# Optimization experiments

Hardware: AMD Instinct MI355X
Metric: run time of the kernel (lower is better)

## Reference

```python
import jax, jax.numpy as jnp
import numpy as np

N_PROJECT = 100000
N_COMPANY = 50000
N_EDGES = 1000000
INPUT_DIM = 256
HIDDEN_DIM = 128
NUM_LAYERS = 2
EPS = 1e-12


def setup_inputs() -> dict:
    key = jax.random.key(0)
    ks = jax.random.split(key, 10)
    return {
        "x_project": jax.random.normal(ks[0], (N_PROJECT, INPUT_DIM), jnp.float32),
        "x_company": jax.random.normal(ks[1], (N_COMPANY, INPUT_DIM), jnp.float32),
        "W_project": jax.random.normal(ks[2], (INPUT_DIM, HIDDEN_DIM), jnp.float32) * 0.05,
        "b_project": jax.random.normal(ks[3], (HIDDEN_DIM,), jnp.float32) * 0.05,
        "W_company": jax.random.normal(ks[4], (INPUT_DIM, HIDDEN_DIM), jnp.float32) * 0.05,
        "b_company": jax.random.normal(ks[5], (HIDDEN_DIM,), jnp.float32) * 0.05,
        "pc_src": jax.random.randint(ks[6], (N_EDGES,), 0, N_PROJECT, jnp.int32),
        "pc_dst": jax.random.randint(ks[7], (N_EDGES,), 0, N_COMPANY, jnp.int32),
        "cp_src": jax.random.randint(ks[8], (N_EDGES,), 0, N_COMPANY, jnp.int32),
        "cp_dst": jax.random.randint(ks[9], (N_EDGES,), 0, N_PROJECT, jnp.int32),
    }


def _rel_aggregate(x_src, row, col, num_src, num_dst):
    # D_src^-1/2 A D_dst^-1/2 normalized gather-scale-scatter_add for one relation.
    ones = jnp.ones(row.shape[0], jnp.float32)
    deg_s = jax.ops.segment_sum(ones, row, num_segments=num_src)
    deg_d = jax.ops.segment_sum(ones, col, num_segments=num_dst)
    inv_s = jnp.where(deg_s > 0, deg_s ** -0.5, 0.0)
    inv_d = jnp.where(deg_d > 0, deg_d ** -0.5, 0.0)
    w = inv_s[row] * inv_d[col]                      # [E]
    msg = x_src[row] * w[:, None]                    # [E, H]
    return jax.ops.segment_sum(msg, col, num_segments=num_dst)  # [num_dst, H]


def reference(x_project, x_company, W_project, b_project, W_company, b_company,
              pc_src, pc_dst, cp_src, cp_dst):
    h_p = x_project @ W_project + b_project          # [Np, H]
    h_c = x_company @ W_company + b_company          # [Nc, H]
    acc_p, acc_c = h_p, h_c
    for _ in range(NUM_LAYERS):
        new_p = _rel_aggregate(h_c, cp_src, cp_dst, N_COMPANY, N_PROJECT)
        new_c = _rel_aggregate(h_p, pc_src, pc_dst, N_PROJECT, N_COMPANY)
        h_p, h_c = new_p, new_c
        acc_p = acc_p + h_p
        acc_c = acc_c + h_c
    scale = 1.0 / (NUM_LAYERS + 1)
    out_p = acc_p * scale
    out_c = acc_c * scale
    # F.normalize(p=2, dim=-1)
    out_p = out_p / jnp.maximum(jnp.linalg.norm(out_p, axis=-1, keepdims=True), EPS)
    out_c = out_c / jnp.maximum(jnp.linalg.norm(out_c, axis=-1, keepdims=True), EPS)
    return out_p, out_c
```

## Files before the change

### kernel.cpp

```cpp
#include <hip/hip_runtime.h>
#include <hip/hip_bf16.h>
#include <math.h>

#define HD 128
#define KD 256
#define CAP 64
#define CAPA 96
#define BA 128

typedef __attribute__((ext_vector_type(8))) short bf16x8;
typedef __attribute__((ext_vector_type(4))) float f32x4;

__device__ __forceinline__ unsigned short bfbits(float x) {
    __hip_bfloat16 h = __float2bfloat16(x);
    return *(unsigned short*)&h;
}
__device__ __forceinline__ unsigned int pack_bf2(float a, float b) {
    __hip_bfloat162 h;
    h.x = __float2bfloat16(a);
    h.y = __float2bfloat16(b);
    return *(unsigned int*)&h;
}
__device__ __forceinline__ float2 unpack_bf2(unsigned int u) {
    __hip_bfloat162 h = *(__hip_bfloat162*)&u;
    return __bfloat1622float2(h);
}
__device__ __forceinline__ bf16x8 cvt8(float4 a, float4 b) {
    bf16x8 r;
    r[0] = (short)bfbits(a.x); r[1] = (short)bfbits(a.y);
    r[2] = (short)bfbits(a.z); r[3] = (short)bfbits(a.w);
    r[4] = (short)bfbits(b.x); r[5] = (short)bfbits(b.y);
    r[6] = (short)bfbits(b.z); r[7] = (short)bfbits(b.w);
    return r;
}

__launch_bounds__(256)
__global__ void phaseA(
        const int* __restrict__ cps, const int* __restrict__ cpd,
        int* __restrict__ db0, int* __restrict__ sb0, int* cntD0, int* cntS0,
        const int* __restrict__ pcs, const int* __restrict__ pcd,
        int* __restrict__ db1, int* __restrict__ sb1, int* cntD1, int* cntS1,
        int E, int G0, int G1,
        const float* __restrict__ WA, unsigned short* __restrict__ WtA,
        const float* __restrict__ WB, unsigned short* __restrict__ WtB) {
    __shared__ int curD[256], curS[256];
    const int b = blockIdx.x;
    if (b >= 2 * BA) {
        int idx = (b - 2 * BA) * 256 + threadIdx.x;
        const float* W = (idx < KD * HD) ? WA : WB;
        unsigned short* Wt = (idx < KD * HD) ? WtA : WtB;
        int id = idx & (KD * HD - 1);
        int j = id & 7, lane = (id >> 3) & 63, nt = (id >> 9) & 7, kc = id >> 12;
        int k = kc * 32 + (lane >> 4) * 8 + j;
        int c = nt * 16 + (lane & 15);
        Wt[id] = bfbits(W[k * HD + c]);
        return;
    }
    const int rel = b >> 7;
    const int ib  = b & (BA - 1);
    const int* src = rel ? pcs : cps;
    const int* dst = rel ? pcd : cpd;
    int* db   = rel ? db1 : db0;
    int* sb   = rel ? sb1 : sb0;
    int* cntD = rel ? cntD1 : cntD0;
    int* cntS = rel ? cntS1 : cntS0;
    const int shD = rel ? 8 : 9;
    const int shS = rel ? 9 : 8;
    const int GD  = rel ? G1 : G0;
    const int GS  = rel ? G0 : G1;

    for (int i = threadIdx.x; i < 256; i += 256) { curD[i] = 0; curS[i] = 0; }
    __syncthreads();

    const int chunk = (E + BA - 1) / BA;
    const int e0 = ib * chunk;
    const int e1 = (e0 + chunk < E) ? e0 + chunk : E;
    for (int e = e0 + (int)threadIdx.x; e < e1; e += 256) {
        const int s = src[e];
        const int d = dst[e];
        const int gd = d >> shD;
        const int pd = atomicAdd(&curD[gd], 1);
        if (pd < CAPA)
            db[((size_t)(ib * GD + gd)) * CAPA + pd] = ((d - (gd << shD)) << 17) | s;
        const int gs = s >> shS;
        const int ps = atomicAdd(&curS[gs], 1);
        if (ps < CAPA)
            sb[((size_t)(ib * GS + gs)) * CAPA + ps] = s;
    }
    __syncthreads();
    for (int g = threadIdx.x; g < GD; g += 256)
        cntD[ib * GD + g] = (curD[g] < CAPA) ? curD[g] : CAPA;
    for (int g = threadIdx.x; g < GS; g += 256)
        cntS[ib * GS + g] = (curS[g] < CAPA) ? curS[g] : CAPA;
}

__device__ __forceinline__ void gemm_body(
        char* smem, const float* __restrict__ X, const unsigned short* __restrict__ Wt,
        const float* __restrict__ bias, unsigned short* __restrict__ out0,
        int M, int tile) {
    float (*eps)[16][68] = (float (*)[16][68])smem;

    const int t = threadIdx.x;
    const int lane = t & 63;
    const int w = t >> 6;
    const int lr = lane & 15;
    const int kb = lane >> 4;
    const int rbase = tile * 128;

    f32x4 acc[2][8];
    #pragma unroll
    for (int nt = 0; nt < 8; ++nt) {
        float bv = bias[nt * 16 + lr];
        acc[0][nt] = (f32x4){bv, bv, bv, bv};
        acc[1][nt] = (f32x4){bv, bv, bv, bv};
    }

    const float4* X4 = (const float4*)X;
    const int r0 = rbase + w * 32 + lr;
    const int r1 = r0 + 16;
    const size_t rr0 = (size_t)((r0 < M) ? r0 : 0) * 64 + kb * 2;
    const size_t rr1 = (size_t)((r1 < M) ? r1 : 0) * 64 + kb * 2;

    float4 xf[2][4];
    #pragma unroll
    for (int s = 0; s < 2; ++s) {
        xf[s][0] = X4[rr0 + s * 8];
        xf[s][1] = X4[rr0 + s * 8 + 1];
        xf[s][2] = X4[rr1 + s * 8];
        xf[s][3] = X4[rr1 + s * 8 + 1];
    }

    #pragma unroll
    for (int kc = 0; kc < 8; ++kc) {
        const int s = kc & 1;
        bf16x8 a0 = cvt8(xf[s][0], xf[s][1]);
        bf16x8 a1 = cvt8(xf[s][2], xf[s][3]);
        if (kc < 6) {
            xf[s][0] = X4[rr0 + (kc + 2) * 8];
            xf[s][1] = X4[rr0 + (kc + 2) * 8 + 1];
            xf[s][2] = X4[rr1 + (kc + 2) * 8];
            xf[s][3] = X4[rr1 + (kc + 2) * 8 + 1];
        }
        const unsigned short* wb = Wt + ((size_t)(kc * 8) * 64 + lane) * 8;
        #pragma unroll
        for (int nt = 0; nt < 8; ++nt) {
            bf16x8 b = *(const bf16x8*)(wb + (size_t)nt * 512);
            acc[0][nt] = __builtin_amdgcn_mfma_f32_16x16x32_bf16(a0, b, acc[0][nt], 0, 0, 0);
            acc[1][nt] = __builtin_amdgcn_mfma_f32_16x16x32_bf16(a1, b, acc[1][nt], 0, 0, 0);
        }
    }

    const int er = lane >> 2;
    const int ec = lane & 3;
    #pragma unroll
    for (int mt = 0; mt < 2; ++mt) {
        #pragma unroll
        for (int hf = 0; hf < 2; ++hf) {
            __syncthreads();
            #pragma unroll
            for (int nt = 0; nt < 4; ++nt)
                #pragma unroll
                for (int reg = 0; reg < 4; ++reg)
                    eps[w][kb * 4 + reg][nt * 16 + lr] = acc[mt][hf * 4 + nt][reg];
            __syncthreads();
            const int g = rbase + w * 32 + mt * 16 + er;
            if (g < M) {
                #pragma unroll
                for (int i = 0; i < 4; ++i) {
                    const int f4c = ec + i * 4;
                    float4 v = *(const float4*)&eps[w][er][f4c * 4];
                    uint2 u;
                    u.x = pack_bf2(v.x, v.y);
                    u.y = pack_bf2(v.z, v.w);
                    *(uint2*)(out0 + (size_t)g * HD + hf * 64 + f4c * 4) = u;
                }
            }
        }
    }
}

__launch_bounds__(256, 4)
__global__ void phaseB(
        const int* __restrict__ db0, const int* cntD0, int* csr0, int* degs0,
        const int* __restrict__ db1, const int* cntD1, int* csr1, int* degs1,
        const int* __restrict__ sb0, const int* cntS0, int* hist0,
        const int* __restrict__ sb1, const int* cntS1, int* hist1,
        int G0, int G1, int Np, int Nc,
        const float* Xp, const unsigned short* WtP, const float* bp,
        unsigned short* h0p, int GP,
        const float* Xc, const unsigned short* WtC, const float* bc,
        unsigned short* h0c) {
    __shared__ __align__(16) char smem[17408];
    int* lcur = (int*)smem;
    const int r = blockIdx.x;
    const int nLight = 2 * (G0 + G1);

    if (r < nLight) {
        int g, sh, GD, M;
        const int *bkt, *cnt;
        int *outp, *degs;
        bool isCSR;
        if (r < G0) {
            g = r; sh = 9; GD = G0; M = Np; bkt = db0; cnt = cntD0;
            outp = csr0; degs = degs0; isCSR = true;
        } else if (r < G0 + G1) {
            g = r - G0; sh = 8; GD = G1; M = Nc; bkt = db1; cnt = cntD1;
            outp = csr1; degs = degs1; isCSR = true;
        } else if (r < G0 + 2 * G1) {
            g = r - G0 - G1; sh = 8; GD = G1; M = Nc; bkt = sb0; cnt = cntS0;
            outp = hist0; degs = hist0; isCSR = false;
        } else {
            g = r - G0 - 2 * G1; sh = 9; GD = G0; M = Np; bkt = sb1; cnt = cntS1;
            outp = hist1; degs = hist1; isCSR = false;
        }
        const int base = g << sh;
        const int rows = ((M - base) < (1 << sh)) ? (M - base) : (1 << sh);
        for (int i = threadIdx.x; i < rows; i += 256) lcur[i] = 0;
        __syncthreads();
        const int total = BA * CAPA;
        if (isCSR) {
            for (int idx = threadIdx.x; idx < total; idx += 256) {
                const int bb = idx / CAPA;
                const int i  = idx - bb * CAPA;
                if (i < cnt[bb * GD + g]) {
                    const unsigned int v = ((const unsigned int*)bkt)[(size_t)(bb * GD + g) * CAPA + i];
                    const int s = (int)(v & 0x1FFFF);
                    const int dloc = (int)(v >> 17);
                    const int p = atomicAdd(&lcur[dloc], 1);
                    if (p < CAP) outp[((size_t)(base + dloc) << 6) + p] = s;
                }
            }
        } else {
            for (int idx = threadIdx.x; idx < total; idx += 256) {
                const int bb = idx / CAPA;
                const int i  = idx - bb * CAPA;
                if (i < cnt[bb * GD + g]) {
                    const int s = bkt[(size_t)(bb * GD + g) * CAPA + i];
                    atomicAdd(&lcur[s - base], 1);
                }
            }
        }
        __syncthreads();
        for (int i = threadIdx.x; i < rows; i += 256)
            degs[base + i] = (lcur[i] < CAP) ? lcur[i] : (isCSR ? CAP : lcur[i]);
        return;
    }

    const int gFlat = r - nLight;
    if (gFlat < GP)
        gemm_body(smem, Xp, WtP, bp, h0p, Np, gFlat);
    else
        gemm_body(smem, Xc, WtC, bc, h0c, Nc, gFlat - GP);
}

__device__ __forceinline__ void agg_gather(const int* __restrict__ degs,
                                           const int* __restrict__ ssrc,
                                           const int* __restrict__ scnt,
                                           const unsigned short* __restrict__ hsrc,
                                           int row, int lane, int q, int cl,
                                           float4& accA, float4& accB) {
    const int deg = degs[row];
    accA = make_float4(0.f, 0.f, 0.f, 0.f);
    accB = make_float4(0.f, 0.f, 0.f, 0.f);
    if (deg > 0) {
        const float id = rsqrtf((float)deg);
        const int n = (deg < CAP) ? deg : CAP;
        int sl = 0; float wl = 0.f;
        if (lane < n) {
            sl = ssrc[((size_t)row << 6) + lane];
            wl = rsqrtf((float)scnt[sl]);
        }
        for (int jj = 0; jj < n; jj += 4) {
            const int j = jj + q;
            const int s = __shfl(sl, j);
            const float wt = __shfl(wl, j) * id;
            const uint4 u = *(const uint4*)(hsrc + (size_t)s * HD + cl * 8);
            const float2 f0 = unpack_bf2(u.x);
            const float2 f1 = unpack_bf2(u.y);
            const float2 f2 = unpack_bf2(u.z);
            const float2 f3 = unpack_bf2(u.w);
            accA.x = fmaf(f0.x, wt, accA.x);
            accA.y = fmaf(f0.y, wt, accA.y);
            accA.z = fmaf(f1.x, wt, accA.z);
            accA.w = fmaf(f1.y, wt, accA.w);
            accB.x = fmaf(f2.x, wt, accB.x);
            accB.y = fmaf(f2.y, wt, accB.y);
            accB.z = fmaf(f3.x, wt, accB.z);
            accB.w = fmaf(f3.y, wt, accB.w);
        }
    }
    accA.x += __shfl_xor(accA.x, 16); accA.y += __shfl_xor(accA.y, 16);
    accA.z += __shfl_xor(accA.z, 16); accA.w += __shfl_xor(accA.w, 16);
    accB.x += __shfl_xor(accB.x, 16); accB.y += __shfl_xor(accB.y, 16);
    accB.z += __shfl_xor(accB.z, 16); accB.w += __shfl_xor(accB.w, 16);
    accA.x += __shfl_xor(accA.x, 32); accA.y += __shfl_xor(accA.y, 32);
    accA.z += __shfl_xor(accA.z, 32); accA.w += __shfl_xor(accA.w, 32);
    accB.x += __shfl_xor(accB.x, 32); accB.y += __shfl_xor(accB.y, 32);
    accB.z += __shfl_xor(accB.z, 32); accB.w += __shfl_xor(accB.w, 32);
}

__global__ void agg_dual(const int* degsA, const int* ssrcA, const int* scntA,
                         const unsigned short* hsrcA, unsigned short* hdstA, int MA,
                         const int* degsB, const int* ssrcB, const int* scntB,
                         const unsigned short* hsrcB, unsigned short* hdstB, int MB) {
    const int bA = (MA + 3) / 4;
    const int lane = threadIdx.x & 63;
    const int q  = lane >> 4;
    const int cl = lane & 15;
    int row;
    const int *degs, *ssrc, *scnt;
    const unsigned short* hsrc; unsigned short* hdst; int M;
    if ((int)blockIdx.x < bA) {
        row = blockIdx.x * 4 + (threadIdx.x >> 6);
        degs = degsA; ssrc = ssrcA; scnt = scntA; hsrc = hsrcA; hdst = hdstA; M = MA;
    } else {
        row = (blockIdx.x - bA) * 4 + (threadIdx.x >> 6);
        degs = degsB; ssrc = ssrcB; scnt = scntB; hsrc = hsrcB; hdst = hdstB; M = MB;
    }
    if (row >= M) return;
    float4 accA, accB;
    agg_gather(degs, ssrc, scnt, hsrc, row, lane, q, cl, accA, accB);
    if (q == 0) {
        uint4 u;
        u.x = pack_bf2(accA.x, accA.y);
        u.y = pack_bf2(accA.z, accA.w);
        u.z = pack_bf2(accB.x, accB.y);
        u.w = pack_bf2(accB.z, accB.w);
        *(uint4*)(hdst + (size_t)row * HD + cl * 8) = u;
    }
}

__global__ void agg_norm_dual(const int* degsA, const int* ssrcA, const int* scntA,
                              const unsigned short* hsrcA, const unsigned short* h0A,
                              const unsigned short* h1A, float* outA, int MA,
                              const int* degsB, const int* ssrcB, const int* scntB,
                              const unsigned short* hsrcB, const unsigned short* h0B,
                              const unsigned short* h1B, float* outB, int MB) {
    const int bA = (MA + 3) / 4;
    const int lane = threadIdx.x & 63;
    const int q  = lane >> 4;
    const int cl = lane & 15;
    int row;
    const int *degs, *ssrc, *scnt;
    const unsigned short *hsrc, *h0, *h1; float* outp; int M;
    if ((int)blockIdx.x < bA) {
        row = blockIdx.x * 4 + (threadIdx.x >> 6);
        degs = degsA; ssrc = ssrcA; scnt = scntA; hsrc = hsrcA;
        h0 = h0A; h1 = h1A; outp = outA; M = MA;
    } else {
        row = (blockIdx.x - bA) * 4 + (threadIdx.x >> 6);
        degs = degsB; ssrc = ssrcB; scnt = scntB; hsrc = hsrcB;
        h0 = h0B; h1 = h1B; outp = outB; M = MB;
    }
    if (row >= M) return;
    float4 accA, accB;
    agg_gather(degs, ssrc, scnt, hsrc, row, lane, q, cl, accA, accB);

    float2 h2;
    if (q == 0)      h2 = make_float2(accA.x, accA.y);
    else if (q == 1) h2 = make_float2(accA.z, accA.w);
    else if (q == 2) h2 = make_float2(accB.x, accB.y);
    else             h2 = make_float2(accB.z, accB.w);

    const int c = cl * 8 + q * 2;
    const size_t base = (size_t)row * HD + c;
    float2 h0v = unpack_bf2(*(const unsigned int*)(h0 + base));
    float2 h1v = unpack_bf2(*(const unsigned int*)(h1 + base));
    const float sc = 1.0f / 3.0f;
    float vx = (h0v.x + h1v.x + h2.x) * sc;
    float vy = (h0v.y + h1v.y + h2.y) * sc;
    float ss = vx * vx + vy * vy;
    #pragma unroll
    for (int off = 1; off < 64; off <<= 1) ss += __shfl_xor(ss, off);
    float inv = 1.0f / fmaxf(sqrtf(ss), 1e-12f);
    *(float2*)(outp + base) = make_float2(vx * inv, vy * inv);
}

extern "C" void kernel_launch(void* const* d_in, const int* in_sizes, int n_in,
                              void* d_out, int out_size, void* d_ws, size_t ws_size,
                              hipStream_t stream) {
    const float* x_p = (const float*)d_in[0];
    const float* x_c = (const float*)d_in[1];
    const float* W_p = (const float*)d_in[2];
    const float* b_p = (const float*)d_in[3];
    const float* W_c = (const float*)d_in[4];
    const float* b_c = (const float*)d_in[5];
    const int* pcs = (const int*)d_in[6];
    const int* pcd = (const int*)d_in[7];
    const int* cps = (const int*)d_in[8];
    const int* cpd = (const int*)d_in[9];

    const int Np = in_sizes[0] / KD;
    const int Nc = in_sizes[1] / KD;
    const int E  = in_sizes[6];

    const int G0 = (Np + 511) >> 9;
    const int G1 = (Nc + 255) >> 8;

    int* scp = (int*)d_ws;
    int* spc = scp + ((size_t)Np << 6);
    int* c_cps = spc + ((size_t)Nc << 6);
    int* c_pcs = c_cps + Nc;
    int* c_cpd = c_pcs + Np;
    int* c_pcd = c_cpd + Np;
    unsigned short* bufP0 = (unsigned short*)(c_pcd + Nc);
    unsigned short* bufP1 = bufP0 + (size_t)Np * HD;
    unsigned short* bufC0 = bufP1 + (size_t)Np * HD;
    unsigned short* bufC1 = bufC0 + (size_t)Nc * HD;
    unsigned short* WtP = bufC1 + (size_t)Nc * HD;
    unsigned short* WtC = WtP + KD * HD;
    int* db0 = (int*)(WtC + KD * HD);
    int* db1 = db0 + (size_t)BA * G0 * CAPA;
    int* sb0 = db1 + (size_t)BA * G1 * CAPA;
    int* sb1 = sb0 + (size_t)BA * G1 * CAPA;
    int* cntD0 = sb1 + (size_t)BA * G0 * CAPA;
    int* cntD1 = cntD0 + BA * G0;
    int* cntS0 = cntD1 + BA * G1;
    int* cntS1 = cntS0 + BA * G1;

    float* outP = (float*)d_out;
    float* outC = outP + (size_t)Np * HD;

    phaseA<<<2 * BA + 256, 256, 0, stream>>>(
        cps, cpd, db0, sb0, cntD0, cntS0,
        pcs, pcd, db1, sb1, cntD1, cntS1,
        E, G0, G1, W_p, WtP, W_c, WtC);

    const int GP = (Np + 127) / 128;
    const int GC = (Nc + 127) / 128;
    phaseB<<<2 * (G0 + G1) + GP + GC, 256, 0, stream>>>(
        db0, cntD0, scp, c_cpd,
        db1, cntD1, spc, c_pcd,
        sb0, cntS0, c_cps,
        sb1, cntS1, c_pcs,
        G0, G1, Np, Nc,
        x_p, WtP, b_p, bufP0, GP,
        x_c, WtC, b_c, bufC0);

    const int bP = (Np + 3) / 4, bC = (Nc + 3) / 4;

    agg_dual<<<bP + bC, 256, 0, stream>>>(
        c_cpd, scp, c_cps, bufC0, bufP1, Np,
        c_pcd, spc, c_pcs, bufP0, bufC1, Nc);

    agg_norm_dual<<<bP + bC, 256, 0, stream>>>(
        c_cpd, scp, c_cps, bufC1, bufP0, bufP1, outP, Np,
        c_pcd, spc, c_pcs, bufP1, bufC0, bufC1, outC, Nc);
}
```

Baseline: 326.4 us.

## Stage full bf16 weight matrix in LDS and prefetch all X rows up front

The GEMM body now copies the entire 256x128 bf16 weight matrix (64 KB) into shared memory per block and reads MFMA B operands from LDS instead of global/L2. All eight K-chunks of X are loaded into registers before the MFMA loop, replacing the two-stage rolling prefetch. Shared memory grows to 64 KB and launch bounds drop to 2 blocks per CU, trading occupancy (also for the light bucket-processing blocks in the same kernel) and register pressure for fewer global weight reads.

```diff
diff --git a/kernel.cpp b/kernel.cpp
--- a/kernel.cpp
+++ b/kernel.cpp
@@ -98,6 +98,8 @@
         char* smem, const float* __restrict__ X, const unsigned short* __restrict__ Wt,
         const float* __restrict__ bias, unsigned short* __restrict__ out0,
         int M, int tile) {
+    uint4* lds4 = (uint4*)smem;
+    const unsigned short* lsh = (const unsigned short*)smem;
     float (*eps)[16][68] = (float (*)[16][68])smem;
 
     const int t = threadIdx.x;
@@ -107,44 +109,41 @@
     const int kb = lane >> 4;
     const int rbase = tile * 128;
 
-    f32x4 acc[2][8];
-    #pragma unroll
-    for (int nt = 0; nt < 8; ++nt) {
-        float bv = bias[nt * 16 + lr];
-        acc[0][nt] = (f32x4){bv, bv, bv, bv};
-        acc[1][nt] = (f32x4){bv, bv, bv, bv};
-    }
+    const uint4* Wg4 = (const uint4*)Wt;
+    #pragma unroll
+    for (int i = 0; i < 16; ++i) { int q = t + i * 256; lds4[q] = Wg4[q]; }
 
     const float4* X4 = (const float4*)X;
     const int r0 = rbase + w * 32 + lr;
     const int r1 = r0 + 16;
     const size_t rr0 = (size_t)((r0 < M) ? r0 : 0) * 64 + kb * 2;
     const size_t rr1 = (size_t)((r1 < M) ? r1 : 0) * 64 + kb * 2;
-
-    float4 xf[2][4];
-    #pragma unroll
-    for (int s = 0; s < 2; ++s) {
-        xf[s][0] = X4[rr0 + s * 8];
-        xf[s][1] = X4[rr0 + s * 8 + 1];
-        xf[s][2] = X4[rr1 + s * 8];
-        xf[s][3] = X4[rr1 + s * 8 + 1];
-    }
-
+    float4 xf[8][4];
     #pragma unroll
     for (int kc = 0; kc < 8; ++kc) {
-        const int s = kc & 1;
-        bf16x8 a0 = cvt8(xf[s][0], xf[s][1]);
-        bf16x8 a1 = cvt8(xf[s][2], xf[s][3]);
-        if (kc < 6) {
-            xf[s][0] = X4[rr0 + (kc + 2) * 8];
-            xf[s][1] = X4[rr0 + (kc + 2) * 8 + 1];
-            xf[s][2] = X4[rr1 + (kc + 2) * 8];
-            xf[s][3] = X4[rr1 + (kc + 2) * 8 + 1];
-        }
-        const unsigned short* wb = Wt + ((size_t)(kc * 8) * 64 + lane) * 8;
+        xf[kc][0] = X4[rr0 + kc * 8];
+        xf[kc][1] = X4[rr0 + kc * 8 + 1];
+        xf[kc][2] = X4[rr1 + kc * 8];
+        xf[kc][3] = X4[rr1 + kc * 8 + 1];
+    }
+
+    f32x4 acc[2][8];
+    #pragma unroll
+    for (int nt = 0; nt < 8; ++nt) {
+        float bv = bias[nt * 16 + lr];
+        acc[0][nt] = (f32x4){bv, bv, bv, bv};
+        acc[1][nt] = (f32x4){bv, bv, bv, bv};
+    }
+
+    __syncthreads();
+
+    #pragma unroll
+    for (int kc = 0; kc < 8; ++kc) {
+        bf16x8 a0 = cvt8(xf[kc][0], xf[kc][1]);
+        bf16x8 a1 = cvt8(xf[kc][2], xf[kc][3]);
         #pragma unroll
         for (int nt = 0; nt < 8; ++nt) {
-            bf16x8 b = *(const bf16x8*)(wb + (size_t)nt * 512);
+            bf16x8 b = *(const bf16x8*)&lsh[(((kc * 8 + nt) * 64) + lane) * 8];
             acc[0][nt] = __builtin_amdgcn_mfma_f32_16x16x32_bf16(a0, b, acc[0][nt], 0, 0, 0);
             acc[1][nt] = __builtin_amdgcn_mfma_f32_16x16x32_bf16(a1, b, acc[1][nt], 0, 0, 0);
         }
@@ -179,7 +178,7 @@
     }
 }
 
-__launch_bounds__(256, 4)
+__launch_bounds__(256, 2)
 __global__ void phaseB(
         const int* __restrict__ db0, const int* cntD0, int* csr0, int* degs0,
         const int* __restrict__ db1, const int* cntD1, int* csr1, int* degs1,
@@ -190,7 +189,7 @@
         unsigned short* h0p, int GP,
         const float* Xc, const unsigned short* WtC, const float* bc,
         unsigned short* h0c) {
-    __shared__ __align__(16) char smem[17408];
+    __shared__ __align__(16) char smem[65536];
     int* lcur = (int*)smem;
     const int r = blockIdx.x;
     const int nLight = 2 * (G0 + G1);
```

After: 322.6 us (median of 3 runs). About the same (-1.2%).

## Overlap projection GEMM with edge bucketing and stage CSR rows in LDS

Applied to the files above, without the earlier changes.

The projection GEMM moves out of the CSR-build kernel into the edge-bucketing kernel, so the dense matmul runs alongside the atomic bucketing work. Weight conversion becomes its own small kernel that runs first. CSR build is now a separate kernel that assembles each 256-row group's neighbour lists in a 64 KB shared-memory tile and writes them out with coalesced 16-byte stores. Both relations now use a uniform 256-row bucket granularity, and the layer-1 feature buffers reuse the bucket scratch memory. In exchange, the per-row neighbour cap drops from 64 to 63, there is one extra launch, and the large LDS footprint limits csrbuild occupancy.

```diff
diff --git a/kernel.cpp b/kernel.cpp
--- a/kernel.cpp
+++ b/kernel.cpp
@@ -34,64 +34,19 @@
     return r;
 }
 
-__launch_bounds__(256)
-__global__ void phaseA(
-        const int* __restrict__ cps, const int* __restrict__ cpd,
-        int* __restrict__ db0, int* __restrict__ sb0, int* cntD0, int* cntS0,
-        const int* __restrict__ pcs, const int* __restrict__ pcd,
-        int* __restrict__ db1, int* __restrict__ sb1, int* cntD1, int* cntS1,
-        int E, int G0, int G1,
-        const float* __restrict__ WA, unsigned short* __restrict__ WtA,
-        const float* __restrict__ WB, unsigned short* __restrict__ WtB) {
-    __shared__ int curD[256], curS[256];
-    const int b = blockIdx.x;
-    if (b >= 2 * BA) {
-        int idx = (b - 2 * BA) * 256 + threadIdx.x;
-        const float* W = (idx < KD * HD) ? WA : WB;
-        unsigned short* Wt = (idx < KD * HD) ? WtA : WtB;
-        int id = idx & (KD * HD - 1);
-        int j = id & 7, lane = (id >> 3) & 63, nt = (id >> 9) & 7, kc = id >> 12;
-        int k = kc * 32 + (lane >> 4) * 8 + j;
-        int c = nt * 16 + (lane & 15);
-        Wt[id] = bfbits(W[k * HD + c]);
-        return;
-    }
-    const int rel = b >> 7;
-    const int ib  = b & (BA - 1);
-    const int* src = rel ? pcs : cps;
-    const int* dst = rel ? pcd : cpd;
-    int* db   = rel ? db1 : db0;
-    int* sb   = rel ? sb1 : sb0;
-    int* cntD = rel ? cntD1 : cntD0;
-    int* cntS = rel ? cntS1 : cntS0;
-    const int shD = rel ? 8 : 9;
-    const int shS = rel ? 9 : 8;
-    const int GD  = rel ? G1 : G0;
-    const int GS  = rel ? G0 : G1;
-
-    for (int i = threadIdx.x; i < 256; i += 256) { curD[i] = 0; curS[i] = 0; }
-    __syncthreads();
-
-    const int chunk = (E + BA - 1) / BA;
-    const int e0 = ib * chunk;
-    const int e1 = (e0 + chunk < E) ? e0 + chunk : E;
-    for (int e = e0 + (int)threadIdx.x; e < e1; e += 256) {
-        const int s = src[e];
-        const int d = dst[e];
-        const int gd = d >> shD;
-        const int pd = atomicAdd(&curD[gd], 1);
-        if (pd < CAPA)
-            db[((size_t)(ib * GD + gd)) * CAPA + pd] = ((d - (gd << shD)) << 17) | s;
-        const int gs = s >> shS;
-        const int ps = atomicAdd(&curS[gs], 1);
-        if (ps < CAPA)
-            sb[((size_t)(ib * GS + gs)) * CAPA + ps] = s;
-    }
-    __syncthreads();
-    for (int g = threadIdx.x; g < GD; g += 256)
-        cntD[ib * GD + g] = (curD[g] < CAPA) ? curD[g] : CAPA;
-    for (int g = threadIdx.x; g < GS; g += 256)
-        cntS[ib * GS + g] = (curS[g] < CAPA) ? curS[g] : CAPA;
+__global__ void convW2(const float* __restrict__ WA, unsigned short* __restrict__ WtA,
+                       const float* __restrict__ WB, unsigned short* __restrict__ WtB) {
+    int idx = blockIdx.x * 256 + threadIdx.x;
+    const float* W = (idx < KD * HD) ? WA : WB;
+    unsigned short* Wt = (idx < KD * HD) ? WtA : WtB;
+    int id = idx & (KD * HD - 1);
+    int j    = id & 7;
+    int lane = (id >> 3) & 63;
+    int nt   = (id >> 9) & 7;
+    int kc   = id >> 12;
+    int k = kc * 32 + (lane >> 4) * 8 + j;
+    int c = nt * 16 + (lane & 15);
+    Wt[id] = bfbits(W[k * HD + c]);
 }
 
 __device__ __forceinline__ void gemm_body(
@@ -180,77 +135,128 @@
 }
 
 __launch_bounds__(256, 4)
-__global__ void phaseB(
+__global__ void fusedAG(
+        const int* __restrict__ cps, const int* __restrict__ cpd,
+        int* __restrict__ db0, int* __restrict__ sb0, int* cntD0, int* cntS0,
+        const int* __restrict__ pcs, const int* __restrict__ pcd,
+        int* __restrict__ db1, int* __restrict__ sb1, int* cntD1, int* cntS1,
+        int E, int G0, int G1,
+        const float* Xp, const unsigned short* WtP, const float* bp,
+        unsigned short* h0p, int Np, int GP,
+        const float* Xc, const unsigned short* WtC, const float* bc,
+        unsigned short* h0c, int Nc) {
+    __shared__ __align__(16) char smem[17408];
+    const int b = blockIdx.x;
+    if (b < 2 * BA) {
+        int* curD = (int*)smem;
+        int* curS = curD + 512;
+        const int rel = b >> 7;
+        const int ib  = b & (BA - 1);
+        const int* src = rel ? pcs : cps;
+        const int* dst = rel ? pcd : cpd;
+        int* db   = rel ? db1 : db0;
+        int* sb   = rel ? sb1 : sb0;
+        int* cntD = rel ? cntD1 : cntD0;
+        int* cntS = rel ? cntS1 : cntS0;
+        const int GD  = rel ? G1 : G0;
+        const int GS  = rel ? G0 : G1;
+
+        for (int i = threadIdx.x; i < 512; i += 256) { curD[i] = 0; curS[i] = 0; }
+        __syncthreads();
+
+        const int chunk = (E + BA - 1) / BA;
+        const int e0 = ib * chunk;
+        const int e1 = (e0 + chunk < E) ? e0 + chunk : E;
+        for (int e = e0 + (int)threadIdx.x; e < e1; e += 256) {
+            const int s = src[e];
+            const int d = dst[e];
+            const int gd = d >> 8;
+            const int pd = atomicAdd(&curD[gd], 1);
+            if (pd < CAPA)
+                db[((size_t)(ib * GD + gd)) * CAPA + pd] = ((d & 255) << 17) | s;
+            const int gs = s >> 8;
+            const int ps = atomicAdd(&curS[gs], 1);
+            if (ps < CAPA)
+                sb[((size_t)(ib * GS + gs)) * CAPA + ps] = s;
+        }
+        __syncthreads();
+        for (int g = threadIdx.x; g < GD; g += 256)
+            cntD[ib * GD + g] = (curD[g] < CAPA) ? curD[g] : CAPA;
+        for (int g = threadIdx.x; g < GS; g += 256)
+            cntS[ib * GS + g] = (curS[g] < CAPA) ? curS[g] : CAPA;
+        return;
+    }
+    const int gFlat = b - 2 * BA;
+    if (gFlat < GP)
+        gemm_body(smem, Xp, WtP, bp, h0p, Np, gFlat);
+    else
+        gemm_body(smem, Xc, WtC, bc, h0c, Nc, gFlat - GP);
+}
+
+__launch_bounds__(256)
+__global__ void csrbuild(
         const int* __restrict__ db0, const int* cntD0, int* csr0, int* degs0,
         const int* __restrict__ db1, const int* cntD1, int* csr1, int* degs1,
         const int* __restrict__ sb0, const int* cntS0, int* hist0,
         const int* __restrict__ sb1, const int* cntS1, int* hist1,
-        int G0, int G1, int Np, int Nc,
-        const float* Xp, const unsigned short* WtP, const float* bp,
-        unsigned short* h0p, int GP,
-        const float* Xc, const unsigned short* WtC, const float* bc,
-        unsigned short* h0c) {
-    __shared__ __align__(16) char smem[17408];
-    int* lcur = (int*)smem;
+        int G0, int G1, int Np, int Nc) {
+    __shared__ int rows[256 * 64];
     const int r = blockIdx.x;
-    const int nLight = 2 * (G0 + G1);
-
-    if (r < nLight) {
-        int g, sh, GD, M;
-        const int *bkt, *cnt;
-        int *outp, *degs;
-        bool isCSR;
-        if (r < G0) {
-            g = r; sh = 9; GD = G0; M = Np; bkt = db0; cnt = cntD0;
-            outp = csr0; degs = degs0; isCSR = true;
-        } else if (r < G0 + G1) {
-            g = r - G0; sh = 8; GD = G1; M = Nc; bkt = db1; cnt = cntD1;
-            outp = csr1; degs = degs1; isCSR = true;
-        } else if (r < G0 + 2 * G1) {
-            g = r - G0 - G1; sh = 8; GD = G1; M = Nc; bkt = sb0; cnt = cntS0;
-            outp = hist0; degs = hist0; isCSR = false;
-        } else {
-            g = r - G0 - 2 * G1; sh = 9; GD = G0; M = Np; bkt = sb1; cnt = cntS1;
-            outp = hist1; degs = hist1; isCSR = false;
-        }
-        const int base = g << sh;
-        const int rows = ((M - base) < (1 << sh)) ? (M - base) : (1 << sh);
-        for (int i = threadIdx.x; i < rows; i += 256) lcur[i] = 0;
-        __syncthreads();
-        const int total = BA * CAPA;
-        if (isCSR) {
-            for (int idx = threadIdx.x; idx < total; idx += 256) {
-                const int bb = idx / CAPA;
-                const int i  = idx - bb * CAPA;
-                if (i < cnt[bb * GD + g]) {
-                    const unsigned int v = ((const unsigned int*)bkt)[(size_t)(bb * GD + g) * CAPA + i];
-                    const int s = (int)(v & 0x1FFFF);
-                    const int dloc = (int)(v >> 17);
-                    const int p = atomicAdd(&lcur[dloc], 1);
-                    if (p < CAP) outp[((size_t)(base + dloc) << 6) + p] = s;
-                }
+    int g, GD, M; const int *bkt, *cnt; int *outp, *degs; bool isCSR;
+    if (r < G0) {
+        g = r; GD = G0; M = Np; bkt = db0; cnt = cntD0;
+        outp = csr0; degs = degs0; isCSR = true;
+    } else if (r < G0 + G1) {
+        g = r - G0; GD = G1; M = Nc; bkt = db1; cnt = cntD1;
+        outp = csr1; degs = degs1; isCSR = true;
+    } else if (r < G0 + 2 * G1) {
+        g = r - G0 - G1; GD = G1; M = Nc; bkt = sb0; cnt = cntS0;
+        outp = hist0; degs = hist0; isCSR = false;
+    } else {
+        g = r - G0 - 2 * G1; GD = G0; M = Np; bkt = sb1; cnt = cntS1;
+        outp = hist1; degs = hist1; isCSR = false;
+    }
+    const int base = g << 8;
+    const int rowsN = ((M - base) < 256) ? (M - base) : 256;
+    const int total = BA * CAPA;
+
+    if (isCSR) {
+        for (int i = threadIdx.x; i < 256; i += 256) rows[(i << 6) + 63] = 0;
+        __syncthreads();
+        for (int idx = threadIdx.x; idx < total; idx += 256) {
+            const int bb = idx / CAPA;
+            const int i  = idx - bb * CAPA;
+            if (i < cnt[bb * GD + g]) {
+                const unsigned int v =
+                    (unsigned int)bkt[((size_t)(bb * GD + g)) * CAPA + i];
+                const int dloc = (int)(v >> 17);
+                const int s = (int)(v & 0x1FFFF);
+                const int p = atomicAdd(&rows[(dloc << 6) + 63], 1);
+                if (p < 63) rows[(dloc << 6) + p] = s;
             }
-        } else {
-            for (int idx = threadIdx.x; idx < total; idx += 256) {
-                const int bb = idx / CAPA;
-                const int i  = idx - bb * CAPA;
-                if (i < cnt[bb * GD + g]) {
-                    const int s = bkt[(size_t)(bb * GD + g) * CAPA + i];
-                    atomicAdd(&lcur[s - base], 1);
-                }
+        }
+        __syncthreads();
+        uint4* dst4 = (uint4*)(outp + ((size_t)base << 6));
+        const uint4* src4 = (const uint4*)rows;
+        for (int q = threadIdx.x; q < rowsN * 16; q += 256) dst4[q] = src4[q];
+        for (int i = threadIdx.x; i < rowsN; i += 256) {
+            const int c = rows[(i << 6) + 63];
+            degs[base + i] = (c < 63) ? c : 63;
+        }
+    } else {
+        for (int i = threadIdx.x; i < 256; i += 256) rows[i] = 0;
+        __syncthreads();
+        for (int idx = threadIdx.x; idx < total; idx += 256) {
+            const int bb = idx / CAPA;
+            const int i  = idx - bb * CAPA;
+            if (i < cnt[bb * GD + g]) {
+                const int s = bkt[((size_t)(bb * GD + g)) * CAPA + i];
+                atomicAdd(&rows[s - base], 1);
             }
         }
         __syncthreads();
-        for (int i = threadIdx.x; i < rows; i += 256)
-            degs[base + i] = (lcur[i] < CAP) ? lcur[i] : (isCSR ? CAP : lcur[i]);
-        return;
-    }
-
-    const int gFlat = r - nLight;
-    if (gFlat < GP)
-        gemm_body(smem, Xp, WtP, bp, h0p, Np, gFlat);
-    else
-        gemm_body(smem, Xc, WtC, bc, h0c, Nc, gFlat - GP);
+        for (int i = threadIdx.x; i < rowsN; i += 256) degs[base + i] = rows[i];
+    }
 }
 
 __device__ __forceinline__ void agg_gather(const int* __restrict__ degs,
@@ -394,7 +400,7 @@
     const int Nc = in_sizes[1] / KD;
     const int E  = in_sizes[6];
 
-    const int G0 = (Np + 511) >> 9;
+    const int G0 = (Np + 255) >> 8;
     const int G1 = (Nc + 255) >> 8;
 
     int* scp = (int*)d_ws;
@@ -404,10 +410,8 @@
     int* c_cpd = c_pcs + Np;
     int* c_pcd = c_cpd + Np;
     unsigned short* bufP0 = (unsigned short*)(c_pcd + Nc);
-    unsigned short* bufP1 = bufP0 + (size_t)Np * HD;
-    unsigned short* bufC0 = bufP1 + (size_t)Np * HD;
-    unsigned short* bufC1 = bufC0 + (size_t)Nc * HD;
-    unsigned short* WtP = bufC1 + (size_t)Nc * HD;
+    unsigned short* bufC0 = bufP0 + (size_t)Np * HD;
+    unsigned short* WtP = bufC0 + (size_t)Nc * HD;
     unsigned short* WtC = WtP + KD * HD;
     int* db0 = (int*)(WtC + KD * HD);
     int* db1 = db0 + (size_t)BA * G0 * CAPA;
@@ -417,25 +421,30 @@
     int* cntD1 = cntD0 + BA * G0;
     int* cntS0 = cntD1 + BA * G1;
     int* cntS1 = cntS0 + BA * G1;
+    unsigned short* bufP1 = (unsigned short*)db0;
+    unsigned short* bufC1 = bufP1 + (size_t)Np * HD;
 
     float* outP = (float*)d_out;
     float* outC = outP + (size_t)Np * HD;
 
-    phaseA<<<2 * BA + 256, 256, 0, stream>>>(
+    const int GP = (Np + 127) / 128;
+    const int GC = (Nc + 127) / 128;
+
+    convW2<<<(2 * KD * HD) / 256, 256, 0, stream>>>(W_p, WtP, W_c, WtC);
+
+    fusedAG<<<2 * BA + GP + GC, 256, 0, stream>>>(
         cps, cpd, db0, sb0, cntD0, cntS0,
         pcs, pcd, db1, sb1, cntD1, cntS1,
-        E, G0, G1, W_p, WtP, W_c, WtC);
-
-    const int GP = (Np + 127) / 128;
-    const int GC = (Nc + 127) / 128;
-    phaseB<<<2 * (G0 + G1) + GP + GC, 256, 0, stream>>>(
+        E, G0, G1,
+        x_p, WtP, b_p, bufP0, Np, GP,
+        x_c, WtC, b_c, bufC0, Nc);
+
+    csrbuild<<<2 * (G0 + G1), 256, 0, stream>>>(
         db0, cntD0, scp, c_cpd,
         db1, cntD1, spc, c_pcd,
         sb0, cntS0, c_cps,
         sb1, cntS1, c_pcs,
-        G0, G1, Np, Nc,
-        x_p, WtP, b_p, bufP0, GP,
-        x_c, WtC, b_c, bufC0);
+        G0, G1, Np, Nc);
 
     const int bP = (Np + 3) / 4, bC = (Nc + 3) / 4;
 
```

Measured after the change: 380.8 us. 1.17x slower.
